# Kernel optimization log

Measured on AMD Instinct MI355X. Metric: run time of the kernel, lower is better.

Reference implementation:

```python
import jax, jax.numpy as jnp
import numpy as np
from jax import lax

CENTER_NUM = 2048


def setup_inputs() -> dict:
    key = jax.random.key(0)
    xyz = jax.random.normal(key, (32, 65536, 3), dtype=jnp.float32)
    return {"xyz": xyz}


def furthest_point_sample(xyz, m):
    """Iterative FPS. xyz: [B, N, 3] -> indices [B, m] (int32).

    Matches pointnet2_utils.furthest_point_sample: start at index 0,
    maintain running min squared distance to the selected set, pick argmax.
    """
    B, N, _ = xyz.shape
    init_idx = jnp.zeros((B,), dtype=jnp.int32)
    init_dists = jnp.full((B, N), 1e10, dtype=xyz.dtype)

    def step(carry, _):
        dists, last_idx = carry
        last = jnp.take_along_axis(xyz, last_idx[:, None, None], axis=1)  # [B,1,3]
        d = jnp.sum((xyz - last) ** 2, axis=-1)  # [B,N] squared dist to last center
        dists = jnp.minimum(dists, d)
        nxt = jnp.argmax(dists, axis=-1).astype(jnp.int32)  # [B]
        return (dists, nxt), nxt

    (_, _), rest = lax.scan(step, (init_dists, init_idx), None, length=m - 1)
    # rest: [m-1, B] -> prepend initial index, transpose to [B, m]
    idx = jnp.concatenate([init_idx[None, :], rest], axis=0).T
    return idx


def index_points(points, idx):
    """points: [B, N, C], idx: [B, m] -> [B, m, C]."""
    return jnp.take_along_axis(points, idx[..., None], axis=1)


def reference(xyz):
    fps_idx = furthest_point_sample(xyz, CENTER_NUM)  # [B, m]
    center_xyz = index_points(xyz, fps_idx)           # [B, m, 3]
    return center_xyz
```

## Files before the change

kernel.cpp:

```cpp
#include <hip/hip_runtime.h>
#include <stdint.h>

#define NBATCH 32
#define NPTS   65536
#define MCENT  2048
#define BPB    8
#define THREADS 1024
#define CHUNK  (NPTS / BPB)
#define WPT    (CHUNK / THREADS)
#define NPAIR  (WPT / 2)
#define NWAVE  (THREADS / 64)
#define GPW    2
#define NGRP   (NWAVE * GPW)
#define TMAX   64

typedef unsigned long long u64;
typedef uint32_t u32;
typedef float v2f __attribute__((ext_vector_type(2)));

static __device__ __forceinline__ u32 fbits(float f) { union { float f; u32 u; } c; c.f = f; return c.u; }
static __device__ __forceinline__ float bitsf(u32 u) { union { u32 u; float f; } c; c.u = u; return c.f; }

static __device__ __forceinline__ u32 wave_max_u32(u32 v) {
#define STEP(CTRL) { const u32 o = (u32)__builtin_amdgcn_update_dpp(0, (int)v, CTRL, 0xF, 0xF, true); v = o > v ? o : v; }
    STEP(0x111)
    STEP(0x112)
    STEP(0x114)
    STEP(0x118)
    STEP(0x142)
    STEP(0x143)
#undef STEP
    return (u32)__builtin_amdgcn_readlane((int)v, 63);
}


template<int TOPK>
__global__ __launch_bounds__(THREADS, 1) void fps_kernel(
    const float* __restrict__ xyz,
    float* __restrict__ out,
    u64* __restrict__ slots)
{
    constexpr int POOLW = BPB * NGRP * TOPK;
    constexpr int WPL   = POOLW / 64;

    const int t = threadIdx.x;
    const int b = blockIdx.x >> 3;
    const int j = blockIdx.x & 7;
    const float* base = xyz + (size_t)b * NPTS * 3;
    const int p0 = j * CHUNK;
    const int wave = t >> 6;
    const int lane = t & 63;

    v2f px2[NPAIR], py2[NPAIR], pz2[NPAIR];
    float pd[WPT];
#pragma unroll
    for (int q = 0; q < WPT; ++q) {
        const int p = p0 + q * THREADS + t;
        px2[q >> 1][q & 1] = base[(size_t)p * 3 + 0];
        py2[q >> 1][q & 1] = base[(size_t)p * 3 + 1];
        pz2[q >> 1][q & 1] = base[(size_t)p * 3 + 2];
        pd[q] = 1e10f;
    }

    __shared__ float wcx[TMAX], wcy[TMAX], wcz[TMAX];
    __shared__ int   wcnt;

    if (t == 0) {
        const float cx = base[0], cy = base[1], cz = base[2];
        wcx[0] = cx; wcy[0] = cy; wcz[0] = cz; wcnt = 1;
        if (j == 0) {
            float* o = out + (size_t)b * MCENT * 3;
            o[0] = cx; o[1] = cy; o[2] = cz;
        }
    }

    int C = 0;
    for (int s = 1; ; ++s) {
        __syncthreads();
        const int tn = wcnt;
        C += tn;
        if (C >= MCENT) break;

        for (int tt = 0; tt < tn; ++tt) {
            const float cx = wcx[tt], cy = wcy[tt], cz = wcz[tt];
            const v2f cx2 = { cx, cx }, cy2 = { cy, cy }, cz2 = { cz, cz };
#pragma unroll
            for (int q = 0; q < NPAIR; ++q) {
                const v2f dx2 = px2[q] - cx2;
                const v2f dy2 = py2[q] - cy2;
                const v2f dz2 = pz2[q] - cz2;
                const v2f t0  = dy2 * dy2;
                const v2f t1  = __builtin_elementwise_fma(dx2, dx2, t0);
                const v2f t2  = __builtin_elementwise_fma(dz2, dz2, t1);
                pd[2 * q + 0] = fminf(pd[2 * q + 0], t2.x);
                pd[2 * q + 1] = fminf(pd[2 * q + 1], t2.y);
            }
        }

        u64 k1 = 0, k2 = 0, k3 = 0;
#pragma unroll
        for (int q = 0; q < WPT; ++q) {
            const u64 kk = ((u64)fbits(pd[q]) << 16)
                         | (u64)(0xFFFFu ^ (u32)(p0 + q * THREADS + t));
            if (kk > k1)      { k3 = k2; k2 = k1; k1 = kk; }
            else if (kk > k2) { k3 = k2; k2 = kk; }
            else if (kk > k3) { k3 = kk; }
        }
#pragma unroll
        for (int m = 1; m <= 16; m <<= 1) {
            const u64 o1 = __shfl_xor(k1, m);
            const u64 o2 = __shfl_xor(k2, m);
            if constexpr (TOPK == 2) {
                if (o1 > k1) { k2 = (k1 > o2) ? k1 : o2; k1 = o1; }
                else         { k2 = (k2 > o1) ? k2 : o1; }
            } else {
                const u64 o3 = __shfl_xor(k3, m);
                u64 m1, m2, m3;
                if (o1 > k1) {
                    m1 = o1;
                    if (o2 > k1) { m2 = o2; m3 = (o3 > k1) ? o3 : k1; }
                    else         { m2 = k1; m3 = (o2 > k2) ? o2 : k2; }
                } else {
                    m1 = k1;
                    if (o1 > k2) { m2 = o1; m3 = (o2 > k2) ? o2 : k2; }
                    else         { m2 = k2; m3 = (o1 > k3) ? o1 : k3; }
                }
                k1 = m1; k2 = m2; k3 = m3;
            }
        }

        u64* const bb = slots + ((size_t)(s & 1) * NBATCH + b) * POOLW;
        const u32 tag = (u32)s & 0xFFFFu;

        if ((lane & 31) == 0) {
            const int g = wave * GPW + (lane >> 5);
            u64* const gw = &bb[j * (NGRP * TOPK) + g * TOPK];
            __hip_atomic_store(&gw[0], (k1 << 16) | tag,
                               __ATOMIC_RELAXED, __HIP_MEMORY_SCOPE_AGENT);
            __hip_atomic_store(&gw[1], (k2 << 16) | tag,
                               __ATOMIC_RELAXED, __HIP_MEMORY_SCOPE_AGENT);
            if constexpr (TOPK == 3)
                __hip_atomic_store(&gw[2], (k3 << 16) | tag,
                                   __ATOMIC_RELAXED, __HIP_MEMORY_SCOPE_AGENT);
        }

        if (wave == 0) {
            u64 w[WPL]; int ok;
            do {
#pragma unroll
                for (int r = 0; r < WPL; ++r)
                    w[r] = __hip_atomic_load(&bb[lane + 64 * r],
                                             __ATOMIC_RELAXED, __HIP_MEMORY_SCOPE_AGENT);
                ok = 1;
#pragma unroll
                for (int r = 0; r < WPL; ++r)
                    ok &= ((u32)(w[r] & 0xFFFFull) == tag);
            } while (!__all(ok));

            u32 pv[WPL], pi[WPL];
            float ex[WPL], ey[WPL], ez[WPL];
#pragma unroll
            for (int r = 0; r < WPL; ++r) {
                pv[r] = (u32)(w[r] >> 32);
                pi[r] = ((u32)w[r] >> 16) & 0xFFFFu;
                const int gi = (int)(0xFFFFu ^ pi[r]);
                ex[r] = base[(size_t)gi * 3 + 0];
                ey[r] = base[(size_t)gi * 3 + 1];
                ez[r] = base[(size_t)gi * 3 + 2];
            }

            u32 tl = 0;
#pragma unroll
            for (int r = 0; r < WPL; ++r) {
                const int rank = ((lane % TOPK) + (64 % TOPK) * r) % TOPK;
                if (rank == TOPK - 1) tl = pv[r] > tl ? pv[r] : tl;
            }
            const u32 tauv = wave_max_u32(tl);

            int tc = 0;
            while (1) {
                u32 lv = 0;
#pragma unroll
                for (int r = 0; r < WPL; ++r) lv = pv[r] > lv ? pv[r] : lv;
                const u32 vmax = wave_max_u32(lv);
                if (tc > 0 && vmax <= tauv) break;

                u32 ic = 0;
#pragma unroll
                for (int r = 0; r < WPL; ++r)
                    ic = (pv[r] == vmax && pi[r] + 1u > ic) ? pi[r] + 1u : ic;
                const u64 bal = __ballot(ic != 0);
                u32 winv; int ol;
                if (__popcll(bal) == 1) {
                    ol = (int)__ffsll((long long)bal) - 1;
                    winv = __shfl(ic, ol) - 1u;
                } else {
                    winv = wave_max_u32(ic) - 1u;
                    int m = 0;
#pragma unroll
                    for (int r = 0; r < WPL; ++r)
                        m |= (pv[r] == vmax) & (pi[r] == winv);
                    ol = (int)__ffsll((long long)__ballot(m)) - 1;
                }

                float sx = 0.f, sy = 0.f, sz = 0.f;
#pragma unroll
                for (int r = 0; r < WPL; ++r) {
                    const int m = (pv[r] == vmax) & (pi[r] == winv);
                    sx = m ? ex[r] : sx;
                    sy = m ? ey[r] : sy;
                    sz = m ? ez[r] : sz;
                }
                const float wx = __shfl(sx, ol);
                const float wy = __shfl(sy, ol);
                const float wz = __shfl(sz, ol);

                if (lane == 0) {
                    wcx[tc] = wx; wcy[tc] = wy; wcz[tc] = wz;
                    if (j == 0) {
                        float* o = out + ((size_t)b * MCENT + (C + tc)) * 3;
                        o[0] = wx; o[1] = wy; o[2] = wz;
                    }
                }
                ++tc;
                if (C + tc >= MCENT || tc >= TMAX) break;

#pragma unroll
                for (int r = 0; r < WPL; ++r) {
                    const float dx = __fsub_rn(ex[r], wx);
                    const float dy = __fsub_rn(ey[r], wy);
                    const float dz = __fsub_rn(ez[r], wz);
                    const float s2 = __fmaf_rn(dz, dz,
                                     __fmaf_rn(dx, dx,
                                     __fmul_rn(dy, dy)));
                    pv[r] = fbits(fminf(bitsf(pv[r]), s2));
                }
            }
            if (lane == 0) wcnt = tc;
        }
    }
}

extern "C" void kernel_launch(void* const* d_in, const int* in_sizes, int n_in,
                              void* d_out, int out_size, void* d_ws, size_t ws_size,
                              hipStream_t stream) {
    const float* xyz = (const float*)d_in[0];
    float* out = (float*)d_out;
    u64* slots = (u64*)d_ws;

    const size_t need3 = 2ull * NBATCH * (BPB * NGRP * 3) * sizeof(u64);
    if (ws_size >= need3) {
        fps_kernel<3><<<dim3(NBATCH * BPB), dim3(THREADS), 0, stream>>>(xyz, out, slots);
    } else {
        fps_kernel<2><<<dim3(NBATCH * BPB), dim3(THREADS), 0, stream>>>(xyz, out, slots);
    }
}
```

Before: 2.087 ms.

## Add spatially sorted FPS kernel with box-bound lower bounds for multi-pick rounds

Adds a new kernel that sorts each block's points by a Morton code, so each 32-lane group holds a spatially compact set, and publishes a per-group bounding box in fp16 with outward rounding. Wave 0 then uses these boxes and each group's third-best value to bound what unseen points could still score. This lets it safely pick more centers per global sync round, where before it stopped once top-3 candidates ran out. The cost is an upfront bitonic sort in shared memory, an extra workspace region and more per-pick work in wave 0. The new path only runs when the workspace is large enough.

```diff
diff --git a/kernel.cpp b/kernel.cpp
--- a/kernel.cpp
+++ b/kernel.cpp
@@ -1,4 +1,5 @@
 #include <hip/hip_runtime.h>
+#include <hip/hip_fp16.h>
 #include <stdint.h>
 
 #define NBATCH 32
@@ -12,10 +13,13 @@
 #define NWAVE  (THREADS / 64)
 #define GPW    2
 #define NGRP   (NWAVE * GPW)
+#define GTOT   (BPB * NGRP)
 #define TMAX   64
+#define BOXTAG 0xBBBBu
 
 typedef unsigned long long u64;
 typedef uint32_t u32;
+typedef uint16_t u16;
 typedef float v2f __attribute__((ext_vector_type(2)));
 
 static __device__ __forceinline__ u32 fbits(float f) { union { float f; u32 u; } c; c.f = f; return c.u; }
@@ -23,16 +27,360 @@
 
 static __device__ __forceinline__ u32 wave_max_u32(u32 v) {
 #define STEP(CTRL) { const u32 o = (u32)__builtin_amdgcn_update_dpp(0, (int)v, CTRL, 0xF, 0xF, true); v = o > v ? o : v; }
-    STEP(0x111)
-    STEP(0x112)
-    STEP(0x114)
-    STEP(0x118)
-    STEP(0x142)
-    STEP(0x143)
+    STEP(0x111) STEP(0x112) STEP(0x114) STEP(0x118) STEP(0x142) STEP(0x143)
 #undef STEP
     return (u32)__builtin_amdgcn_readlane((int)v, 63);
 }
-
+static __device__ __forceinline__ void wave_max2_u32(u32 &a, u32 &b) {
+#define STEP2(CTRL) { const u32 oa = (u32)__builtin_amdgcn_update_dpp(0, (int)a, CTRL, 0xF, 0xF, true); \
+                      const u32 ob = (u32)__builtin_amdgcn_update_dpp(0, (int)b, CTRL, 0xF, 0xF, true); \
+                      a = oa > a ? oa : a; b = ob > b ? ob : b; }
+    STEP2(0x111) STEP2(0x112) STEP2(0x114) STEP2(0x118) STEP2(0x142) STEP2(0x143)
+#undef STEP2
+    a = (u32)__builtin_amdgcn_readlane((int)a, 63);
+    b = (u32)__builtin_amdgcn_readlane((int)b, 63);
+}
+
+static __device__ __forceinline__ u16 h_down(float x) {
+    __half h = __float2half(x); float f = __half2float(h);
+    u16 bb = __half_as_ushort(h);
+    if (f > x) { if (bb == 0x0000u) bb = 0x8001u; else if (bb & 0x8000u) bb += 1; else bb -= 1; }
+    return bb;
+}
+static __device__ __forceinline__ u16 h_up(float x) {
+    __half h = __float2half(x); float f = __half2float(h);
+    u16 bb = __half_as_ushort(h);
+    if (f < x) { if (bb == 0x8000u) bb = 0x0001u; else if (bb & 0x8000u) bb -= 1; else bb += 1; }
+    return bb;
+}
+static __device__ __forceinline__ u32 spread4(int v) {
+    return (u32)((v & 1) | ((v & 2) << 2) | ((v & 4) << 4) | ((v & 8) << 6));
+}
+
+__global__ __launch_bounds__(THREADS, 1) void fps_spatial(
+    const float* __restrict__ xyz,
+    float* __restrict__ out,
+    u64* __restrict__ slots)
+{
+    constexpr int TOPK  = 3;
+    constexpr int POOLW = BPB * NGRP * TOPK;
+    constexpr int WPL   = POOLW / 64;
+
+    const int t = threadIdx.x;
+    const int b = blockIdx.x >> 3;
+    const int j = blockIdx.x & 7;
+    const float* base = xyz + (size_t)b * NPTS * 3;
+    const int p0 = j * CHUNK;
+    const int wave = t >> 6;
+    const int lane = t & 63;
+
+    __shared__ u32   skey[CHUNK];
+    __shared__ float boxf[GTOT * 6];
+    __shared__ float wcx[TMAX], wcy[TMAX], wcz[TMAX];
+    __shared__ int   wcnt;
+    __shared__ float red[6 * NWAVE];
+
+    float mnx = 3e38f, mny = 3e38f, mnz = 3e38f;
+    float mxx = -3e38f, mxy = -3e38f, mxz = -3e38f;
+    for (int q = 0; q < WPT; ++q) {
+        const int p = p0 + q * THREADS + t;
+        const float x = base[(size_t)p * 3 + 0];
+        const float y = base[(size_t)p * 3 + 1];
+        const float z = base[(size_t)p * 3 + 2];
+        mnx = fminf(mnx, x); mxx = fmaxf(mxx, x);
+        mny = fminf(mny, y); mxy = fmaxf(mxy, y);
+        mnz = fminf(mnz, z); mxz = fmaxf(mxz, z);
+    }
+#pragma unroll
+    for (int m = 1; m <= 32; m <<= 1) {
+        mnx = fminf(mnx, __shfl_xor(mnx, m)); mxx = fmaxf(mxx, __shfl_xor(mxx, m));
+        mny = fminf(mny, __shfl_xor(mny, m)); mxy = fmaxf(mxy, __shfl_xor(mxy, m));
+        mnz = fminf(mnz, __shfl_xor(mnz, m)); mxz = fmaxf(mxz, __shfl_xor(mxz, m));
+    }
+    if (lane == 0) {
+        red[wave] = mnx; red[NWAVE + wave] = mny; red[2 * NWAVE + wave] = mnz;
+        red[3 * NWAVE + wave] = mxx; red[4 * NWAVE + wave] = mxy; red[5 * NWAVE + wave] = mxz;
+    }
+    __syncthreads();
+    mnx = red[0]; mny = red[NWAVE]; mnz = red[2 * NWAVE];
+    mxx = red[3 * NWAVE]; mxy = red[4 * NWAVE]; mxz = red[5 * NWAVE];
+    for (int i = 1; i < NWAVE; ++i) {
+        mnx = fminf(mnx, red[i]); mny = fminf(mny, red[NWAVE + i]); mnz = fminf(mnz, red[2 * NWAVE + i]);
+        mxx = fmaxf(mxx, red[3 * NWAVE + i]); mxy = fmaxf(mxy, red[4 * NWAVE + i]); mxz = fmaxf(mxz, red[5 * NWAVE + i]);
+    }
+    const float sx = 16.0f / (mxx - mnx + 1e-20f);
+    const float sy = 16.0f / (mxy - mny + 1e-20f);
+    const float sz = 16.0f / (mxz - mnz + 1e-20f);
+    __syncthreads();
+
+    for (int q = 0; q < WPT; ++q) {
+        const int li = q * THREADS + t;
+        const int p = p0 + li;
+        const float x = base[(size_t)p * 3 + 0];
+        const float y = base[(size_t)p * 3 + 1];
+        const float z = base[(size_t)p * 3 + 2];
+        int qx = (int)((x - mnx) * sx); qx = qx < 0 ? 0 : (qx > 15 ? 15 : qx);
+        int qy = (int)((y - mny) * sy); qy = qy < 0 ? 0 : (qy > 15 ? 15 : qy);
+        int qz = (int)((z - mnz) * sz); qz = qz < 0 ? 0 : (qz > 15 ? 15 : qz);
+        const u32 m12 = spread4(qx) | (spread4(qy) << 1) | (spread4(qz) << 2);
+        skey[li] = (m12 << 13) | (u32)li;
+    }
+    __syncthreads();
+
+    for (int k = 2; k <= CHUNK; k <<= 1) {
+        for (int jj = k >> 1; jj >= 1; jj >>= 1) {
+            for (int q = 0; q < WPT; ++q) {
+                const int i = q * THREADS + t;
+                const int ix = i ^ jj;
+                if (ix > i) {
+                    const u32 a = skey[i], c = skey[ix];
+                    const bool up = ((i & k) == 0);
+                    if ((a > c) == up) { skey[i] = c; skey[ix] = a; }
+                }
+            }
+            __syncthreads();
+        }
+    }
+
+    v2f px2[NPAIR], py2[NPAIR], pz2[NPAIR];
+    float pd[WPT];
+    u32 invp[WPT];
+    for (int q = 0; q < WPT; ++q) {
+        const int slot = t * WPT + q;
+        const int li = (int)(skey[slot] & 0x1FFFu);
+        const int p = p0 + li;
+        px2[q >> 1][q & 1] = base[(size_t)p * 3 + 0];
+        py2[q >> 1][q & 1] = base[(size_t)p * 3 + 1];
+        pz2[q >> 1][q & 1] = base[(size_t)p * 3 + 2];
+        pd[q] = 1e10f;
+        invp[q] = 0xFFFFu ^ (u32)p;
+    }
+
+    float blx = 3e38f, bly = 3e38f, blz = 3e38f;
+    float bhx = -3e38f, bhy = -3e38f, bhz = -3e38f;
+#pragma unroll
+    for (int q = 0; q < WPT; ++q) {
+        const float x = px2[q >> 1][q & 1], y = py2[q >> 1][q & 1], z = pz2[q >> 1][q & 1];
+        blx = fminf(blx, x); bhx = fmaxf(bhx, x);
+        bly = fminf(bly, y); bhy = fmaxf(bhy, y);
+        blz = fminf(blz, z); bhz = fmaxf(bhz, z);
+    }
+#pragma unroll
+    for (int m = 1; m <= 16; m <<= 1) {
+        blx = fminf(blx, __shfl_xor(blx, m)); bhx = fmaxf(bhx, __shfl_xor(bhx, m));
+        bly = fminf(bly, __shfl_xor(bly, m)); bhy = fmaxf(bhy, __shfl_xor(bhy, m));
+        blz = fminf(blz, __shfl_xor(blz, m)); bhz = fmaxf(bhz, __shfl_xor(bhz, m));
+    }
+    u64* const boxw = slots + (size_t)2 * NBATCH * POOLW + (size_t)b * (GTOT * 2);
+    if ((lane & 31) == 0) {
+        const int g = j * NGRP + wave * GPW + (lane >> 5);
+        const u64 lo = ((u64)h_down(blx)) | ((u64)h_down(bly) << 16) | ((u64)h_down(blz) << 32);
+        const u64 hi = ((u64)h_up(bhx))  | ((u64)h_up(bhy)  << 16) | ((u64)h_up(bhz)  << 32);
+        __hip_atomic_store(&boxw[g * 2 + 0], (lo << 16) | BOXTAG, __ATOMIC_RELAXED, __HIP_MEMORY_SCOPE_AGENT);
+        __hip_atomic_store(&boxw[g * 2 + 1], (hi << 16) | BOXTAG, __ATOMIC_RELAXED, __HIP_MEMORY_SCOPE_AGENT);
+    }
+    if (t == 0) {
+        const float cx = base[0], cy = base[1], cz = base[2];
+        wcx[0] = cx; wcy[0] = cy; wcz[0] = cz; wcnt = 1;
+        if (j == 0) {
+            float* o = out + (size_t)b * MCENT * 3;
+            o[0] = cx; o[1] = cy; o[2] = cz;
+        }
+    }
+    if (wave == 0) {
+        u64 v[8]; int ok;
+        do {
+#pragma unroll
+            for (int r = 0; r < 8; ++r)
+                v[r] = __hip_atomic_load(&boxw[lane + 64 * r], __ATOMIC_RELAXED, __HIP_MEMORY_SCOPE_AGENT);
+            ok = 1;
+#pragma unroll
+            for (int r = 0; r < 8; ++r) ok &= ((u32)(v[r] & 0xFFFFull) == BOXTAG);
+        } while (!__all(ok));
+#pragma unroll
+        for (int r = 0; r < 8; ++r) {
+            const int wi = lane + 64 * r;
+            const u64 pay = v[r] >> 16;
+            const int g = wi >> 1, half = wi & 1;
+            boxf[g * 6 + half * 3 + 0] = __half2float(__ushort_as_half((u16)(pay & 0xFFFFu)));
+            boxf[g * 6 + half * 3 + 1] = __half2float(__ushort_as_half((u16)((pay >> 16) & 0xFFFFu)));
+            boxf[g * 6 + half * 3 + 2] = __half2float(__ushort_as_half((u16)((pay >> 32) & 0xFFFFu)));
+        }
+    }
+
+    int C = 0;
+    for (int s = 1; ; ++s) {
+        __syncthreads();
+        const int tn = wcnt;
+        C += tn;
+        if (C >= MCENT) break;
+
+        for (int tt = 0; tt < tn; ++tt) {
+            const float cx = wcx[tt], cy = wcy[tt], cz = wcz[tt];
+            const v2f cx2 = { cx, cx }, cy2 = { cy, cy }, cz2 = { cz, cz };
+#pragma unroll
+            for (int q = 0; q < NPAIR; ++q) {
+                const v2f dx2 = px2[q] - cx2;
+                const v2f dy2 = py2[q] - cy2;
+                const v2f dz2 = pz2[q] - cz2;
+                const v2f t0 = dy2 * dy2;
+                const v2f t1 = __builtin_elementwise_fma(dx2, dx2, t0);
+                const v2f t2 = __builtin_elementwise_fma(dz2, dz2, t1);
+                pd[2 * q + 0] = fminf(pd[2 * q + 0], t2.x);
+                pd[2 * q + 1] = fminf(pd[2 * q + 1], t2.y);
+            }
+        }
+
+        u64 k1 = 0, k2 = 0, k3 = 0;
+#pragma unroll
+        for (int q = 0; q < WPT; ++q) {
+            const u64 kk = ((u64)fbits(pd[q]) << 16) | (u64)invp[q];
+            if (kk > k1)      { k3 = k2; k2 = k1; k1 = kk; }
+            else if (kk > k2) { k3 = k2; k2 = kk; }
+            else if (kk > k3) { k3 = kk; }
+        }
+#pragma unroll
+        for (int m = 1; m <= 16; m <<= 1) {
+            const u64 o1 = __shfl_xor(k1, m);
+            const u64 o2 = __shfl_xor(k2, m);
+            const u64 o3 = __shfl_xor(k3, m);
+            u64 m1, m2, m3;
+            if (o1 > k1) {
+                m1 = o1;
+                if (o2 > k1) { m2 = o2; m3 = (o3 > k1) ? o3 : k1; }
+                else         { m2 = k1; m3 = (o2 > k2) ? o2 : k2; }
+            } else {
+                m1 = k1;
+                if (o1 > k2) { m2 = o1; m3 = (o2 > k2) ? o2 : k2; }
+                else         { m2 = k2; m3 = (o1 > k3) ? o1 : k3; }
+            }
+            k1 = m1; k2 = m2; k3 = m3;
+        }
+
+        u64* const bb = slots + ((size_t)(s & 1) * NBATCH + b) * POOLW;
+        const u32 tag = (u32)s & 0xFFFFu;
+
+        if ((lane & 31) == 0) {
+            const int g = wave * GPW + (lane >> 5);
+            u64* const gw = &bb[j * (NGRP * TOPK) + g * TOPK];
+            __hip_atomic_store(&gw[0], (k1 << 16) | tag, __ATOMIC_RELAXED, __HIP_MEMORY_SCOPE_AGENT);
+            __hip_atomic_store(&gw[1], (k2 << 16) | tag, __ATOMIC_RELAXED, __HIP_MEMORY_SCOPE_AGENT);
+            __hip_atomic_store(&gw[2], (k3 << 16) | tag, __ATOMIC_RELAXED, __HIP_MEMORY_SCOPE_AGENT);
+        }
+
+        if (wave == 0) {
+            u64 w[WPL]; int ok;
+            do {
+#pragma unroll
+                for (int r = 0; r < WPL; ++r)
+                    w[r] = __hip_atomic_load(&bb[lane + 64 * r], __ATOMIC_RELAXED, __HIP_MEMORY_SCOPE_AGENT);
+                ok = 1;
+#pragma unroll
+                for (int r = 0; r < WPL; ++r)
+                    ok &= ((u32)(w[r] & 0xFFFFull) == tag);
+            } while (!__all(ok));
+
+            u32 pv[WPL], pi[WPL];
+            float ex[WPL], ey[WPL], ez[WPL];
+#pragma unroll
+            for (int r = 0; r < WPL; ++r) {
+                pv[r] = (u32)(w[r] >> 32);
+                pi[r] = ((u32)w[r] >> 16) & 0xFFFFu;
+                const int gi = (int)(0xFFFFu ^ pi[r]);
+                ex[r] = base[(size_t)gi * 3 + 0];
+                ey[r] = base[(size_t)gi * 3 + 1];
+                ez[r] = base[(size_t)gi * 3 + 2];
+            }
+
+            u32 third[4]; float cr[4];
+#pragma unroll
+            for (int i = 0; i < 4; ++i) {
+                const u64 tw = __hip_atomic_load(&bb[(4 * lane + i) * 3 + 2],
+                                                 __ATOMIC_RELAXED, __HIP_MEMORY_SCOPE_AGENT);
+                third[i] = (u32)(tw >> 32);
+                cr[i] = 3e38f;
+            }
+            u32 lb = 0;
+#pragma unroll
+            for (int i = 0; i < 4; ++i) lb = third[i] > lb ? third[i] : lb;
+
+            int tc = 0;
+            while (1) {
+                u32 lv = 0;
+#pragma unroll
+                for (int r = 0; r < WPL; ++r) lv = pv[r] > lv ? pv[r] : lv;
+                u32 vmax = lv, tau = lb;
+                wave_max2_u32(vmax, tau);
+                if (tc > 0 && vmax <= tau) break;
+
+                u32 ic = 0;
+#pragma unroll
+                for (int r = 0; r < WPL; ++r)
+                    ic = (pv[r] == vmax && pi[r] + 1u > ic) ? pi[r] + 1u : ic;
+                const u64 bal = __ballot(ic != 0);
+                u32 winv; int ol;
+                if (__popcll(bal) == 1) {
+                    ol = (int)__ffsll((long long)bal) - 1;
+                    winv = __shfl(ic, ol) - 1u;
+                } else {
+                    winv = wave_max_u32(ic) - 1u;
+                    int m = 0;
+#pragma unroll
+                    for (int r = 0; r < WPL; ++r)
+                        m |= (pv[r] == vmax) & (pi[r] == winv);
+                    ol = (int)__ffsll((long long)__ballot(m)) - 1;
+                }
+                float sxc = 0.f, syc = 0.f, szc = 0.f;
+#pragma unroll
+                for (int r = 0; r < WPL; ++r) {
+                    const int m = (pv[r] == vmax) & (pi[r] == winv);
+                    sxc = m ? ex[r] : sxc;
+                    syc = m ? ey[r] : syc;
+                    szc = m ? ez[r] : szc;
+                }
+                const float wx = __shfl(sxc, ol);
+                const float wy = __shfl(syc, ol);
+                const float wz = __shfl(szc, ol);
+
+                if (lane == 0) {
+                    wcx[tc] = wx; wcy[tc] = wy; wcz[tc] = wz;
+                    if (j == 0) {
+                        float* o = out + ((size_t)b * MCENT + (C + tc)) * 3;
+                        o[0] = wx; o[1] = wy; o[2] = wz;
+                    }
+                }
+                ++tc;
+                if (C + tc >= MCENT || tc >= TMAX) break;
+
+#pragma unroll
+                for (int r = 0; r < WPL; ++r) {
+                    const float dx = __fsub_rn(ex[r], wx);
+                    const float dy = __fsub_rn(ey[r], wy);
+                    const float dz = __fsub_rn(ez[r], wz);
+                    const float s2 = __fmaf_rn(dz, dz,
+                                     __fmaf_rn(dx, dx,
+                                     __fmul_rn(dy, dy)));
+                    pv[r] = fbits(fminf(bitsf(pv[r]), s2));
+                }
+                u32 nlb = 0;
+#pragma unroll
+                for (int i = 0; i < 4; ++i) {
+                    const int gg = 4 * lane + i;
+                    const float mx = fmaxf(wx - boxf[gg * 6 + 0], boxf[gg * 6 + 3] - wx);
+                    const float my = fmaxf(wy - boxf[gg * 6 + 1], boxf[gg * 6 + 4] - wy);
+                    const float mz = fmaxf(wz - boxf[gg * 6 + 2], boxf[gg * 6 + 5] - wz);
+                    const float md2 = __fmaf_rn(mz, mz, __fmaf_rn(my, my, __fmul_rn(mx, mx)));
+                    cr[i] = fminf(cr[i], md2);
+                    const u32 cb = fbits(cr[i]);
+                    const u32 bi = third[i] < cb ? third[i] : cb;
+                    nlb = bi > nlb ? bi : nlb;
+                }
+                lb = nlb;
+            }
+            if (lane == 0) wcnt = tc;
+        }
+    }
+}
 
 template<int TOPK>
 __global__ __launch_bounds__(THREADS, 1) void fps_kernel(
@@ -89,9 +437,9 @@
                 const v2f dx2 = px2[q] - cx2;
                 const v2f dy2 = py2[q] - cy2;
                 const v2f dz2 = pz2[q] - cz2;
-                const v2f t0  = dy2 * dy2;
-                const v2f t1  = __builtin_elementwise_fma(dx2, dx2, t0);
-                const v2f t2  = __builtin_elementwise_fma(dz2, dz2, t1);
+                const v2f t0 = dy2 * dy2;
+                const v2f t1 = __builtin_elementwise_fma(dx2, dx2, t0);
+                const v2f t2 = __builtin_elementwise_fma(dz2, dz2, t1);
                 pd[2 * q + 0] = fminf(pd[2 * q + 0], t2.x);
                 pd[2 * q + 1] = fminf(pd[2 * q + 1], t2.y);
             }
@@ -135,13 +483,10 @@
         if ((lane & 31) == 0) {
             const int g = wave * GPW + (lane >> 5);
             u64* const gw = &bb[j * (NGRP * TOPK) + g * TOPK];
-            __hip_atomic_store(&gw[0], (k1 << 16) | tag,
-                               __ATOMIC_RELAXED, __HIP_MEMORY_SCOPE_AGENT);
-            __hip_atomic_store(&gw[1], (k2 << 16) | tag,
-                               __ATOMIC_RELAXED, __HIP_MEMORY_SCOPE_AGENT);
+            __hip_atomic_store(&gw[0], (k1 << 16) | tag, __ATOMIC_RELAXED, __HIP_MEMORY_SCOPE_AGENT);
+            __hip_atomic_store(&gw[1], (k2 << 16) | tag, __ATOMIC_RELAXED, __HIP_MEMORY_SCOPE_AGENT);
             if constexpr (TOPK == 3)
-                __hip_atomic_store(&gw[2], (k3 << 16) | tag,
-                                   __ATOMIC_RELAXED, __HIP_MEMORY_SCOPE_AGENT);
+                __hip_atomic_store(&gw[2], (k3 << 16) | tag, __ATOMIC_RELAXED, __HIP_MEMORY_SCOPE_AGENT);
         }
 
         if (wave == 0) {
@@ -149,8 +494,7 @@
             do {
 #pragma unroll
                 for (int r = 0; r < WPL; ++r)
-                    w[r] = __hip_atomic_load(&bb[lane + 64 * r],
-                                             __ATOMIC_RELAXED, __HIP_MEMORY_SCOPE_AGENT);
+                    w[r] = __hip_atomic_load(&bb[lane + 64 * r], __ATOMIC_RELAXED, __HIP_MEMORY_SCOPE_AGENT);
                 ok = 1;
 #pragma unroll
                 for (int r = 0; r < WPL; ++r)
@@ -203,17 +547,17 @@
                     ol = (int)__ffsll((long long)__ballot(m)) - 1;
                 }
 
-                float sx = 0.f, sy = 0.f, sz = 0.f;
+                float sxc = 0.f, syc = 0.f, szc = 0.f;
 #pragma unroll
                 for (int r = 0; r < WPL; ++r) {
                     const int m = (pv[r] == vmax) & (pi[r] == winv);
-                    sx = m ? ex[r] : sx;
-                    sy = m ? ey[r] : sy;
-                    sz = m ? ez[r] : sz;
-                }
-                const float wx = __shfl(sx, ol);
-                const float wy = __shfl(sy, ol);
-                const float wz = __shfl(sz, ol);
+                    sxc = m ? ex[r] : sxc;
+                    syc = m ? ey[r] : syc;
+                    szc = m ? ez[r] : szc;
+                }
+                const float wx = __shfl(sxc, ol);
+                const float wy = __shfl(syc, ol);
+                const float wz = __shfl(szc, ol);
 
                 if (lane == 0) {
                     wcx[tc] = wx; wcy[tc] = wy; wcz[tc] = wz;
@@ -248,8 +592,12 @@
     float* out = (float*)d_out;
     u64* slots = (u64*)d_ws;
 
-    const size_t need3 = 2ull * NBATCH * (BPB * NGRP * 3) * sizeof(u64);
-    if (ws_size >= need3) {
+    const size_t need_sp = (size_t)2 * NBATCH * (BPB * NGRP * 3) * sizeof(u64)
+                         + (size_t)NBATCH * (GTOT * 2) * sizeof(u64);
+    const size_t need3 = (size_t)2 * NBATCH * (BPB * NGRP * 3) * sizeof(u64);
+    if (ws_size >= need_sp) {
+        fps_spatial<<<dim3(NBATCH * BPB), dim3(THREADS), 0, stream>>>(xyz, out, slots);
+    } else if (ws_size >= need3) {
         fps_kernel<3><<<dim3(NBATCH * BPB), dim3(THREADS), 0, stream>>>(xyz, out, slots);
     } else {
         fps_kernel<2><<<dim3(NBATCH * BPB), dim3(THREADS), 0, stream>>>(xyz, out, slots);
```

Result: slower. 3.283 ms (+57.4%).
